# Performance work log

Measured on AMD Instinct MI355X. Metric: run time of the kernel, lower is better.

## Reference

```python
import jax, jax.numpy as jnp
import numpy as np

V = 20000; FV = 2000; PV = 31
SE = 400; FE = 50; PE = 5; NE = 5
FR = FE + PE + NE  # 60, field_rep_embed_size
H = 512; HH = H // 2  # decoder hidden, encoder per-direction hidden
B = 32; T = 32; S = 100
TE = 300  # target_lookup dim (hardcoded in module)


def setup_inputs() -> dict:
    key = jax.random.key(0)
    ks = jax.random.split(key, 26)
    g = lambda k, shape, s: (jax.random.normal(k, shape, jnp.float32) * s)
    inp = {}
    inp['sent'] = jax.random.randint(ks[0], (B, T), 0, V)
    inp['value'] = jax.random.randint(ks[1], (B, S), 0, V)
    inp['field'] = jax.random.randint(ks[2], (B, S), 0, FV)
    inp['ppos'] = jax.random.randint(ks[3], (B, S), 0, PV)
    inp['pneg'] = jax.random.randint(ks[4], (B, S), 0, PV)
    inp['batch_size'] = B
    inp['value_mask'] = jnp.ones((B, S), jnp.float32)
    inp['align_prob'] = jax.random.uniform(ks[5], (B, S, V), jnp.float32)
    # embedding tables
    inp['sent_emb'] = g(ks[6], (V, SE), 0.05)
    inp['field_emb'] = g(ks[7], (FV, FE), 0.05)
    inp['ppos_emb'] = g(ks[8], (PV, PE), 0.05)
    inp['pneg_emb'] = g(ks[9], (PV, NE), 0.05)
    inp['target_emb'] = g(ks[10], (V, TE), 0.05)
    # bidirectional encoder LSTM (per-direction hidden HH), torch gate order i,f,g,o
    ein = SE + FR
    inp['Wi_f'] = g(ks[11], (ein, 4 * HH), ein ** -0.5)
    inp['Wh_f'] = g(ks[12], (HH, 4 * HH), HH ** -0.5)
    inp['b_f'] = jnp.zeros((4 * HH,), jnp.float32)
    inp['Wi_b'] = g(ks[13], (ein, 4 * HH), ein ** -0.5)
    inp['Wh_b'] = g(ks[14], (HH, 4 * HH), HH ** -0.5)
    inp['b_b'] = jnp.zeros((4 * HH,), jnp.float32)
    # decoder LSTM cell + dual attention params
    inp['Wi_d'] = g(ks[15], (SE, 4 * H), SE ** -0.5)
    inp['Wh_d'] = g(ks[16], (H, 4 * H), H ** -0.5)
    inp['b_d'] = jnp.zeros((4 * H,), jnp.float32)
    inp['Wa'] = g(ks[17], (H, H), H ** -0.5)   # encoder-state attention proj
    inp['Wf'] = g(ks[18], (FR, H), FR ** -0.5) # field-rep attention proj
    inp['Wo'] = g(ks[19], (2 * H, H), (2 * H) ** -0.5)  # output proj [h;ctx]
    inp['Wl'] = g(ks[20], (2 * H + SE, 1), (2 * H + SE) ** -0.5)  # lamda gate
    inp['bl'] = jnp.zeros((1,), jnp.float32)
    # linear_out: encoder_hidden_size -> vocab
    inp['Wout'] = g(ks[21], (H, V), H ** -0.5)
    inp['bout'] = jnp.zeros((V,), jnp.float32)
    return inp


def _cell(x, h, c, Wi, Wh, b):
    z = x @ Wi + h @ Wh + b
    i, f, g, o = jnp.split(z, 4, axis=-1)
    c = jax.nn.sigmoid(f) * c + jax.nn.sigmoid(i) * jnp.tanh(g)
    h = jax.nn.sigmoid(o) * jnp.tanh(c)
    return h, c


def _run_lstm(xseq, Wi, Wh, b):
    # xseq [B,L,E] -> hs [B,L,Hn], (hT, cT)
    Bn = xseq.shape[0]; Hn = Wh.shape[0]
    init = (jnp.zeros((Bn, Hn), xseq.dtype), jnp.zeros((Bn, Hn), xseq.dtype))
    def step(carry, xt):
        h, c = _cell(xt, carry[0], carry[1], Wi, Wh, b)
        return (h, c), h
    (hT, cT), hs = jax.lax.scan(step, init, jnp.swapaxes(xseq, 0, 1))
    return jnp.swapaxes(hs, 0, 1), hT, cT


def reference(sent, value, field, ppos, pneg, batch_size, value_mask, align_prob,
              sent_emb, field_emb, ppos_emb, pneg_emb, target_emb,
              Wi_f, Wh_f, b_f, Wi_b, Wh_b, b_b,
              Wi_d, Wh_d, b_d, Wa, Wf, Wo, Wl, bl, Wout, bout):
    # --- encoder input: word emb of table values + field/pos/neg-pos embs ---
    input_d = sent_emb[value]                                     # [B,S,SE]
    input_z = jnp.concatenate([field_emb[field], ppos_emb[ppos], pneg_emb[pneg]], axis=2)  # [B,S,FR]
    enc_in = jnp.concatenate([input_d, input_z], axis=2)          # [B,S,SE+FR]
    # bidirectional LSTM (dropout is eval-mode identity)
    hs_f, hTf, cTf = _run_lstm(enc_in, Wi_f, Wh_f, b_f)
    hs_b, hTb, cTb = _run_lstm(enc_in[:, ::-1], Wi_b, Wh_b, b_b)
    enc_out = jnp.concatenate([hs_f, hs_b[:, ::-1]], axis=-1)     # [B,S,H]
    h0 = jnp.concatenate([hTf, hTb], axis=-1)                     # [B,H]
    c0 = jnp.concatenate([cTf, cTb], axis=-1)

    # --- dual-attention decoder ---
    x_seq = sent_emb[sent]                                        # [B,T,SE]
    enc_proj = jnp.einsum('bsh,hk->bsk', enc_out, Wa)             # word-level keys
    z_proj = jnp.einsum('bsf,fk->bsk', input_z, Wf)               # field-level keys

    def dstep(carry, xt):
        h, c = _cell(xt, carry[0], carry[1], Wi_d, Wh_d, b_d)
        alpha = jax.nn.softmax(jnp.einsum('bsh,bh->bs', enc_proj, h), axis=-1)
        beta = jax.nn.softmax(jnp.einsum('bsh,bh->bs', z_proj, h), axis=-1)
        g = alpha * beta
        g = g / (jnp.sum(g, axis=-1, keepdims=True) + 1e-9)       # dual attn weights
        ctx = jnp.einsum('bs,bsh->bh', g, enc_out)
        out = jnp.tanh(jnp.concatenate([h, ctx], axis=-1) @ Wo)   # [B,H]
        lam = jax.nn.sigmoid(jnp.concatenate([h, ctx, xt], axis=-1) @ Wl + bl)  # [B,1]
        return (h, c), (out, g, lam)

    (hT, cT), (outs, attn, lam) = jax.lax.scan(dstep, (h0, c0), jnp.swapaxes(x_seq, 0, 1))
    outs = jnp.swapaxes(outs, 0, 1)   # [B,T,H]
    attn = jnp.swapaxes(attn, 0, 1)   # [B,T,S]
    lam = jnp.swapaxes(lam, 0, 1)     # [B,T,1]

    p_mod = jax.nn.log_softmax(outs @ Wout + bout, axis=2)        # [B,T,V]
    p_lex = jnp.einsum('bts,bsv->btv', attn, align_prob)          # bmm
    p_bias = jax.nn.log_softmax(lam * p_lex + (1.0 - lam) * p_mod, axis=2)

    # position_idx_to_value: vectorized gather replacing the scalar double loop
    max_idx_attn = jnp.argmax(attn, axis=2)                       # [B,T]
    word_idx = jnp.take_along_axis(value, max_idx_attn, axis=1)   # [B,T]
    attn_pred = target_emb[word_idx]                              # [B,T,300]
    decoder_pred = target_emb[jnp.argmax(p_bias, axis=2)]         # [B,T,300]
    return p_bias, (hT, cT), attn_pred, decoder_pred
```

## Files before the change

kernel.cpp:

```cpp
#include <hip/hip_runtime.h>
#include <cstdint>
#include <cstddef>

static constexpr int Bn  = 32;
static constexpr int Tn  = 32;
static constexpr int Sn  = 100;
static constexpr int Vn  = 20000;
static constexpr int SEn = 400;
static constexpr int EINn= 460;
static constexpr int Hn  = 512;
static constexpr int HHn = 256;
static constexpr int TEn = 300;

__device__ __forceinline__ float sigm(float x) { return 1.f / (1.f + expf(-x)); }

__global__ __launch_bounds__(256) void embed_kernel(
    const int* __restrict__ value, const int* __restrict__ field,
    const int* __restrict__ ppos, const int* __restrict__ pneg,
    const int* __restrict__ sent,
    const float* __restrict__ sent_emb, const float* __restrict__ field_emb,
    const float* __restrict__ ppos_emb, const float* __restrict__ pneg_emb,
    float* __restrict__ enc_in, float* __restrict__ x_seq)
{
    int i = blockIdx.x * 256 + threadIdx.x;
    const int total1 = Bn * Sn * EINn;
    if (i < total1) {
        int e = i % EINn, bs = i / EINn;
        float v;
        if (e < SEn)      v = sent_emb[(size_t)value[bs] * SEn + e];
        else if (e < 450) v = field_emb[field[bs] * 50 + (e - 400)];
        else if (e < 455) v = ppos_emb[ppos[bs] * 5 + (e - 450)];
        else              v = pneg_emb[pneg[bs] * 5 + (e - 455)];
        enc_in[i] = v;
    } else {
        int i2 = i - total1;
        if (i2 < Bn * Tn * SEn) {
            int e = i2 % SEn, bt = i2 / SEn;
            x_seq[i2] = sent_emb[(size_t)sent[bt] * SEn + e];
        }
    }
}

__global__ __launch_bounds__(256) void gemm128_kernel(
    const float* __restrict__ A, const float* __restrict__ Bm,
    const float* __restrict__ bias, float* __restrict__ C,
    int M, int N, int K, int lda, int ldb, int ldc)
{
    __shared__ float As[8][128];
    __shared__ float Bs[8][128];
    const int bm = blockIdx.y * 128, bn = blockIdx.x * 128;
    const int tid = threadIdx.x;
    const int tx = tid & 15, ty = tid >> 4;
    const int row0 = ty * 8, col0 = tx * 8;
    float acc[8][8] = {};
    for (int k0 = 0; k0 < K; k0 += 8) {
        #pragma unroll
        for (int i = 0; i < 4; ++i) {
            int idx = tid + 256 * i;
            int m = idx >> 3, kk = idx & 7;
            float v = 0.f;
            if (bm + m < M && k0 + kk < K) v = A[(size_t)(bm + m) * lda + (k0 + kk)];
            As[kk][m] = v;
        }
        #pragma unroll
        for (int i = 0; i < 4; ++i) {
            int idx = tid + 256 * i;
            int kk = idx >> 7, n = idx & 127;
            float v = 0.f;
            if (k0 + kk < K && bn + n < N) v = Bm[(size_t)(k0 + kk) * ldb + (bn + n)];
            Bs[kk][n] = v;
        }
        __syncthreads();
        #pragma unroll
        for (int kk = 0; kk < 8; ++kk) {
            float a[8], b[8];
            #pragma unroll
            for (int i = 0; i < 8; ++i) a[i] = As[kk][row0 + i];
            #pragma unroll
            for (int j = 0; j < 8; ++j) b[j] = Bs[kk][col0 + j];
            #pragma unroll
            for (int i = 0; i < 8; ++i)
                #pragma unroll
                for (int j = 0; j < 8; ++j) acc[i][j] = fmaf(a[i], b[j], acc[i][j]);
        }
        __syncthreads();
    }
    #pragma unroll
    for (int i = 0; i < 8; ++i) {
        int m = bm + row0 + i;
        if (m >= M) continue;
        #pragma unroll
        for (int j = 0; j < 8; ++j) {
            int n = bn + col0 + j;
            if (n < N) {
                float v = acc[i][j];
                if (bias) v += bias[n];
                C[(size_t)m * ldc + n] = v;
            }
        }
    }
}

__global__ __launch_bounds__(1024) void enc_lstm_kernel(
    const float* __restrict__ Xf, const float* __restrict__ Xb,
    const float* __restrict__ Whf, const float* __restrict__ Whb,
    float* __restrict__ enc_out, float* __restrict__ h0, float* __restrict__ c0)
{
    const int b = blockIdx.x >> 1, dir = blockIdx.x & 1;
    const float* __restrict__ X  = dir ? Xb : Xf;
    const float* __restrict__ Wh = dir ? Whb : Whf;
    __shared__ float h_sh[HHn];
    __shared__ float z_sh[4 * HHn];
    const int u = threadIdx.x;
    float c = 0.f;
    if (u < HHn) h_sh[u] = 0.f;
    __syncthreads();
    for (int step = 0; step < Sn; ++step) {
        const int s = dir ? (Sn - 1 - step) : step;
        const float* xrow = X + ((size_t)b * Sn + s) * 1024;
        float z = xrow[u];
        #pragma unroll 4
        for (int k = 0; k < HHn; ++k)
            z = fmaf(h_sh[k], Wh[k * 1024 + u], z);
        z_sh[u] = z;
        __syncthreads();
        if (u < HHn) {
            float zi = z_sh[u], zf = z_sh[HHn + u], zg = z_sh[2 * HHn + u], zo = z_sh[3 * HHn + u];
            c = sigm(zf) * c + sigm(zi) * tanhf(zg);
            float h = sigm(zo) * tanhf(c);
            h_sh[u] = h;
            enc_out[((size_t)b * Sn + s) * Hn + dir * HHn + u] = h;
            if (step == Sn - 1) {
                h0[b * Hn + dir * HHn + u] = h;
                c0[b * Hn + dir * HHn + u] = c;
            }
        }
        __syncthreads();
    }
}

__global__ __launch_bounds__(1024) void dec_lstm_kernel(
    const float* __restrict__ Xd, const float* __restrict__ Whd,
    const float* __restrict__ h0, const float* __restrict__ c0,
    float* __restrict__ h_all, float* __restrict__ hT, float* __restrict__ cT)
{
    const int b = blockIdx.x;
    __shared__ float h_sh[Hn];
    __shared__ float z_sh[4 * Hn];
    const int u = threadIdx.x;
    float c = 0.f;
    if (u < Hn) { h_sh[u] = h0[b * Hn + u]; c = c0[b * Hn + u]; }
    __syncthreads();
    for (int t = 0; t < Tn; ++t) {
        const float* xrow = Xd + ((size_t)b * Tn + t) * 2048;
        float z0 = xrow[u], z1 = xrow[1024 + u];
        #pragma unroll 4
        for (int k = 0; k < Hn; ++k) {
            float hk = h_sh[k];
            z0 = fmaf(hk, Whd[(size_t)k * 2048 + u], z0);
            z1 = fmaf(hk, Whd[(size_t)k * 2048 + 1024 + u], z1);
        }
        z_sh[u] = z0; z_sh[1024 + u] = z1;
        __syncthreads();
        if (u < Hn) {
            float zi = z_sh[u], zf = z_sh[Hn + u], zg = z_sh[2 * Hn + u], zo = z_sh[3 * Hn + u];
            c = sigm(zf) * c + sigm(zi) * tanhf(zg);
            float h = sigm(zo) * tanhf(c);
            h_sh[u] = h;
            h_all[((size_t)b * Tn + t) * Hn + u] = h;
            if (t == Tn - 1) { hT[b * Hn + u] = h; cT[b * Hn + u] = c; }
        }
        __syncthreads();
    }
}

__global__ __launch_bounds__(256) void dec_post_kernel(
    const float* __restrict__ h_all, const float* __restrict__ enc_proj,
    const float* __restrict__ z_proj, const float* __restrict__ enc_out,
    const float* __restrict__ x_seq, const float* __restrict__ Wo,
    const float* __restrict__ Wl, const float* __restrict__ bl,
    const int* __restrict__ value, const float* __restrict__ target_emb,
    float* __restrict__ outs, float* __restrict__ gattn,
    float* __restrict__ lamv, float* __restrict__ attn_pred)
{
    const int bt = blockIdx.x, b = bt >> 5;
    const int tid = threadIdx.x;
    __shared__ float h_sh[Hn];
    __shared__ float sc[2 * Sn];
    __shared__ float g_sh[Sn];
    __shared__ float ctx_sh[Hn];
    __shared__ float red[256];
    __shared__ int smax_sh;

    for (int i = tid; i < Hn; i += 256) h_sh[i] = h_all[(size_t)bt * Hn + i];
    __syncthreads();

    const int wave = tid >> 6, lane = tid & 63;
    for (int s = wave; s < Sn; s += 4) {
        const float* ep = enc_proj + ((size_t)b * Sn + s) * Hn;
        const float* zp = z_proj  + ((size_t)b * Sn + s) * Hn;
        float da = 0.f, db = 0.f;
        for (int j = lane; j < Hn; j += 64) {
            float hv = h_sh[j];
            da = fmaf(ep[j], hv, da);
            db = fmaf(zp[j], hv, db);
        }
        #pragma unroll
        for (int off = 32; off; off >>= 1) {
            da += __shfl_down(da, off);
            db += __shfl_down(db, off);
        }
        if (lane == 0) { sc[s] = da; sc[Sn + s] = db; }
    }
    __syncthreads();

    if (tid == 0) {
        float ma = -1e30f, mb = -1e30f;
        for (int s = 0; s < Sn; ++s) { ma = fmaxf(ma, sc[s]); mb = fmaxf(mb, sc[Sn + s]); }
        float sa = 0.f, sb = 0.f;
        for (int s = 0; s < Sn; ++s) {
            float ea = expf(sc[s] - ma), eb = expf(sc[Sn + s] - mb);
            sc[s] = ea; sc[Sn + s] = eb; sa += ea; sb += eb;
        }
        float gs = 0.f;
        for (int s = 0; s < Sn; ++s) { float g = (sc[s] / sa) * (sc[Sn + s] / sb); g_sh[s] = g; gs += g; }
        float inv = 1.f / (gs + 1e-9f);
        float best = -1.f; int bi = 0;
        for (int s = 0; s < Sn; ++s) {
            float g = g_sh[s] * inv; g_sh[s] = g;
            if (g > best) { best = g; bi = s; }
        }
        smax_sh = bi;
    }
    __syncthreads();

    for (int s = tid; s < Sn; s += 256) gattn[(size_t)bt * Sn + s] = g_sh[s];
    const int word = value[b * Sn + smax_sh];
    for (int e = tid; e < TEn; e += 256)
        attn_pred[(size_t)bt * TEn + e] = target_emb[(size_t)word * TEn + e];

    for (int u = tid; u < Hn; u += 256) {
        float acc = 0.f;
        for (int s = 0; s < Sn; ++s)
            acc = fmaf(g_sh[s], enc_out[((size_t)b * Sn + s) * Hn + u], acc);
        ctx_sh[u] = acc;
    }
    __syncthreads();

    for (int j = tid; j < Hn; j += 256) {
        float acc = 0.f;
        for (int k = 0; k < Hn; ++k) acc = fmaf(h_sh[k], Wo[(size_t)k * Hn + j], acc);
        for (int k = 0; k < Hn; ++k) acc = fmaf(ctx_sh[k], Wo[(size_t)(Hn + k) * Hn + j], acc);
        outs[(size_t)bt * Hn + j] = tanhf(acc);
    }

    float part = 0.f;
    for (int k = tid; k < Hn; k += 256) part = fmaf(h_sh[k], Wl[k], part);
    for (int k = tid; k < Hn; k += 256) part = fmaf(ctx_sh[k], Wl[Hn + k], part);
    const float* xr = x_seq + (size_t)bt * SEn;
    for (int k = tid; k < SEn; k += 256) part = fmaf(xr[k], Wl[2 * Hn + k], part);
    red[tid] = part;
    __syncthreads();
    for (int s2 = 128; s2; s2 >>= 1) {
        if (tid < s2) red[tid] += red[tid + s2];
        __syncthreads();
    }
    if (tid == 0) lamv[bt] = 1.f / (1.f + expf(-(red[0] + bl[0])));
}

__global__ __launch_bounds__(256) void p_lex_kernel(
    const float* __restrict__ gattn, const float* __restrict__ align_prob,
    float* __restrict__ p_lex)
{
    const int b = blockIdx.z, th = blockIdx.y, vc = blockIdx.x;
    const int tid = threadIdx.x;
    __shared__ float gT[Sn][17];
    for (int i = tid; i < Sn * 16; i += 256) {
        int s = i >> 4, tt = i & 15;
        gT[s][tt] = gattn[((size_t)(b * Tn + th * 16 + tt)) * Sn + s];
    }
    __syncthreads();
    const int v0 = vc * 1024 + tid * 4;
    if (v0 >= Vn) return;
    float acc[16][4] = {};
    for (int s = 0; s < Sn; ++s) {
        const float4 a = *(const float4*)(align_prob + ((size_t)b * Sn + s) * Vn + v0);
        #pragma unroll
        for (int tt = 0; tt < 16; ++tt) {
            float g = gT[s][tt];
            acc[tt][0] = fmaf(g, a.x, acc[tt][0]);
            acc[tt][1] = fmaf(g, a.y, acc[tt][1]);
            acc[tt][2] = fmaf(g, a.z, acc[tt][2]);
            acc[tt][3] = fmaf(g, a.w, acc[tt][3]);
        }
    }
    #pragma unroll
    for (int tt = 0; tt < 16; ++tt) {
        float4 o;
        o.x = acc[tt][0]; o.y = acc[tt][1]; o.z = acc[tt][2]; o.w = acc[tt][3];
        *(float4*)(p_lex + ((size_t)(b * Tn + th * 16 + tt)) * Vn + v0) = o;
    }
}

__global__ __launch_bounds__(256) void reduce1_kernel(
    const float* __restrict__ z, float* __restrict__ lse1)
{
    const int r = blockIdx.x, tid = threadIdx.x;
    const float* row = z + (size_t)r * Vn;
    __shared__ float red[256];
    float m = -1e30f;
    for (int v = tid; v < Vn; v += 256) m = fmaxf(m, row[v]);
    red[tid] = m; __syncthreads();
    for (int s = 128; s; s >>= 1) { if (tid < s) red[tid] = fmaxf(red[tid], red[tid + s]); __syncthreads(); }
    m = red[0]; __syncthreads();
    float sum = 0.f;
    for (int v = tid; v < Vn; v += 256) sum += expf(row[v] - m);
    red[tid] = sum; __syncthreads();
    for (int s = 128; s; s >>= 1) { if (tid < s) red[tid] += red[tid + s]; __syncthreads(); }
    if (tid == 0) lse1[r] = m + logf(red[0]);
}

__global__ __launch_bounds__(256) void combine_kernel(
    float* __restrict__ q, const float* __restrict__ p_lex,
    const float* __restrict__ lamv, const float* __restrict__ lse1,
    float* __restrict__ lse2, int* __restrict__ amax)
{
    const int r = blockIdx.x, tid = threadIdx.x;
    const float l = lamv[r], ls1 = lse1[r];
    float* row = q + (size_t)r * Vn;
    const float* pl = p_lex + (size_t)r * Vn;
    __shared__ float rm[256];
    __shared__ int ri[256];
    float m = -1e30f; int mi = 0;
    for (int v = tid; v < Vn; v += 256) {
        float qq = l * pl[v] + (1.f - l) * (row[v] - ls1);
        row[v] = qq;
        if (qq > m) { m = qq; mi = v; }
    }
    rm[tid] = m; ri[tid] = mi; __syncthreads();
    for (int s = 128; s; s >>= 1) {
        if (tid < s) {
            if (rm[tid + s] > rm[tid] || (rm[tid + s] == rm[tid] && ri[tid + s] < ri[tid])) {
                rm[tid] = rm[tid + s]; ri[tid] = ri[tid + s];
            }
        }
        __syncthreads();
    }
    m = rm[0];
    const int best = ri[0];
    __syncthreads();
    float sum = 0.f;
    for (int v = tid; v < Vn; v += 256) sum += expf(row[v] - m);
    rm[tid] = sum; __syncthreads();
    for (int s = 128; s; s >>= 1) { if (tid < s) rm[tid] += rm[tid + s]; __syncthreads(); }
    if (tid == 0) { lse2[r] = m + logf(rm[0]); amax[r] = best; }
}

__global__ __launch_bounds__(256) void finalize_kernel(
    float* __restrict__ pbias, const float* __restrict__ lse2,
    const int* __restrict__ amax, const float* __restrict__ target_emb,
    float* __restrict__ dec_pred)
{
    const int r = blockIdx.x, tid = threadIdx.x;
    const float ls = lse2[r];
    float* row = pbias + (size_t)r * Vn;
    for (int v = tid; v < Vn; v += 256) row[v] -= ls;
    const int wd = amax[r];
    for (int e = tid; e < TEn; e += 256)
        dec_pred[(size_t)r * TEn + e] = target_emb[(size_t)wd * TEn + e];
}

extern "C" void kernel_launch(void* const* d_in, const int* in_sizes, int n_in,
                              void* d_out, int out_size, void* d_ws, size_t ws_size,
                              hipStream_t stream)
{
    const int*   sent       = (const int*)d_in[0];
    const int*   value      = (const int*)d_in[1];
    const int*   field      = (const int*)d_in[2];
    const int*   ppos       = (const int*)d_in[3];
    const int*   pneg       = (const int*)d_in[4];
    const float* align_prob = (const float*)d_in[7];
    const float* sent_emb   = (const float*)d_in[8];
    const float* field_emb  = (const float*)d_in[9];
    const float* ppos_emb   = (const float*)d_in[10];
    const float* pneg_emb   = (const float*)d_in[11];
    const float* target_emb = (const float*)d_in[12];
    const float* Wi_f = (const float*)d_in[13];
    const float* Wh_f = (const float*)d_in[14];
    const float* b_f  = (const float*)d_in[15];
    const float* Wi_b = (const float*)d_in[16];
    const float* Wh_b = (const float*)d_in[17];
    const float* b_b  = (const float*)d_in[18];
    const float* Wi_d = (const float*)d_in[19];
    const float* Wh_d = (const float*)d_in[20];
    const float* b_d  = (const float*)d_in[21];
    const float* Wa   = (const float*)d_in[22];
    const float* Wf   = (const float*)d_in[23];
    const float* Wo   = (const float*)d_in[24];
    const float* Wl   = (const float*)d_in[25];
    const float* bl   = (const float*)d_in[26];
    const float* Wout = (const float*)d_in[27];
    const float* bout = (const float*)d_in[28];

    float* w = (float*)d_ws;
    float* enc_in   = w; w += (size_t)Bn * Sn * EINn;
    float* x_seq    = w; w += (size_t)Bn * Tn * SEn;
    float* Xf       = w; w += (size_t)Bn * Sn * 1024;
    float* Xb       = w; w += (size_t)Bn * Sn * 1024;
    float* Xd       = w; w += (size_t)Bn * Tn * 2048;
    float* enc_out  = w; w += (size_t)Bn * Sn * Hn;
    float* enc_proj = w; w += (size_t)Bn * Sn * Hn;
    float* z_proj   = w; w += (size_t)Bn * Sn * Hn;
    float* h0       = w; w += (size_t)Bn * Hn;
    float* c0       = w; w += (size_t)Bn * Hn;
    float* h_all    = w; w += (size_t)Bn * Tn * Hn;
    float* outs     = w; w += (size_t)Bn * Tn * Hn;
    float* gattn    = w; w += (size_t)Bn * Tn * Sn;
    float* lamv     = w; w += (size_t)Bn * Tn;
    float* p_lex    = w; w += (size_t)Bn * Tn * Vn;
    float* lse1     = w; w += (size_t)Bn * Tn;
    float* lse2     = w; w += (size_t)Bn * Tn;
    int*   amax     = (int*)w;

    float* outp      = (float*)d_out;
    float* pbias     = outp;
    float* hT        = outp + (size_t)20480000;
    float* cT        = hT + Bn * Hn;
    float* attn_pred = cT + Bn * Hn;
    float* dec_pred  = attn_pred + (size_t)Bn * Tn * TEn;

    embed_kernel<<<7350, 256, 0, stream>>>(value, field, ppos, pneg, sent,
        sent_emb, field_emb, ppos_emb, pneg_emb, enc_in, x_seq);

    dim3 gXf(8, 25);
    gemm128_kernel<<<gXf, 256, 0, stream>>>(enc_in, Wi_f, b_f, Xf, 3200, 1024, 460, 460, 1024, 1024);
    gemm128_kernel<<<gXf, 256, 0, stream>>>(enc_in, Wi_b, b_b, Xb, 3200, 1024, 460, 460, 1024, 1024);
    dim3 gXd(16, 8);
    gemm128_kernel<<<gXd, 256, 0, stream>>>(x_seq, Wi_d, b_d, Xd, 1024, 2048, 400, 400, 2048, 2048);

    enc_lstm_kernel<<<64, 1024, 0, stream>>>(Xf, Xb, Wh_f, Wh_b, enc_out, h0, c0);

    dim3 gPr(4, 25);
    gemm128_kernel<<<gPr, 256, 0, stream>>>(enc_out, Wa, nullptr, enc_proj, 3200, 512, 512, 512, 512, 512);
    gemm128_kernel<<<gPr, 256, 0, stream>>>(enc_in + 400, Wf, nullptr, z_proj, 3200, 512, 60, 460, 512, 512);

    dec_lstm_kernel<<<32, 1024, 0, stream>>>(Xd, Wh_d, h0, c0, h_all, hT, cT);

    dec_post_kernel<<<1024, 256, 0, stream>>>(h_all, enc_proj, z_proj, enc_out, x_seq,
        Wo, Wl, bl, value, target_emb, outs, gattn, lamv, attn_pred);

    dim3 gBig(157, 8);
    gemm128_kernel<<<gBig, 256, 0, stream>>>(outs, Wout, bout, pbias, 1024, 20000, 512, 512, 20000, 20000);

    dim3 gPl(20, 2, 32);
    p_lex_kernel<<<gPl, 256, 0, stream>>>(gattn, align_prob, p_lex);

    reduce1_kernel<<<1024, 256, 0, stream>>>(pbias, lse1);
    combine_kernel<<<1024, 256, 0, stream>>>(pbias, p_lex, lamv, lse1, lse2, amax);
    finalize_kernel<<<1024, 256, 0, stream>>>(pbias, lse2, amax, target_emb, dec_pred);

    (void)in_sizes; (void)n_in; (void)out_size; (void)ws_size;
}
```

Before: 4.923 ms.

## Interleave LSTM recurrent weights per unit and split decoder LSTM across blocks

Recurrent weight matrices are transposed once per call into a per-unit float4 layout holding the i,f,g,o gate columns, so each thread computes all four gates of one unit and applies the cell update without a shared-memory gate exchange. Both LSTM kernels drop from 1024 to 256 threads per block. The decoder is spread over two cooperative blocks per batch row that swap h through a global buffer and a grid-wide atomic barrier every step. This adds a transpose kernel, a memset and spin-barrier latency per step, and stores the scratch weights in the p_lex workspace region before that region is written.

```diff
diff --git a/kernel.cpp b/kernel.cpp
--- a/kernel.cpp
+++ b/kernel.cpp
@@ -13,6 +13,12 @@
 static constexpr int TEn = 300;
 
 __device__ __forceinline__ float sigm(float x) { return 1.f / (1.f + expf(-x)); }
+
+__device__ __forceinline__ void fma4(float hk, const float4 w,
+                                     float& zi, float& zf, float& zg, float& zo) {
+    zi = fmaf(hk, w.x, zi); zf = fmaf(hk, w.y, zf);
+    zg = fmaf(hk, w.z, zg); zo = fmaf(hk, w.w, zo);
+}
 
 __global__ __launch_bounds__(256) void embed_kernel(
     const int* __restrict__ value, const int* __restrict__ field,
@@ -41,6 +47,33 @@
     }
 }
 
+__global__ __launch_bounds__(256) void transpose_wh_kernel(
+    const float* __restrict__ Whf, const float* __restrict__ Whb,
+    const float* __restrict__ Whd,
+    float* __restrict__ Whf_t, float* __restrict__ Whb_t, float* __restrict__ Whd_t)
+{
+    int i = blockIdx.x * 256 + threadIdx.x;
+    if (i < 65536) {
+        int k = i >> 8, u = i & 255;
+        const float* p = Whf + (size_t)k * 1024 + u;
+        float4 o;
+        o.x = p[0]; o.y = p[256]; o.z = p[512]; o.w = p[768];
+        *(float4*)(Whf_t + (size_t)i * 4) = o;
+        p = Whb + (size_t)k * 1024 + u;
+        o.x = p[0]; o.y = p[256]; o.z = p[512]; o.w = p[768];
+        *(float4*)(Whb_t + (size_t)i * 4) = o;
+    } else {
+        int j = i - 65536;
+        if (j < 262144) {
+            int k = j >> 9, u = j & 511;
+            const float* p = Whd + (size_t)k * 2048 + u;
+            float4 o;
+            o.x = p[0]; o.y = p[512]; o.z = p[1024]; o.w = p[1536];
+            *(float4*)(Whd_t + (size_t)j * 4) = o;
+        }
+    }
+}
+
 __global__ __launch_bounds__(256) void gemm128_kernel(
     const float* __restrict__ A, const float* __restrict__ Bm,
     const float* __restrict__ bias, float* __restrict__ C,
@@ -101,75 +134,93 @@
     }
 }
 
-__global__ __launch_bounds__(1024) void enc_lstm_kernel(
+__global__ __launch_bounds__(256) void enc_lstm2_kernel(
     const float* __restrict__ Xf, const float* __restrict__ Xb,
-    const float* __restrict__ Whf, const float* __restrict__ Whb,
+    const float4* __restrict__ Whf_t, const float4* __restrict__ Whb_t,
     float* __restrict__ enc_out, float* __restrict__ h0, float* __restrict__ c0)
 {
     const int b = blockIdx.x >> 1, dir = blockIdx.x & 1;
-    const float* __restrict__ X  = dir ? Xb : Xf;
-    const float* __restrict__ Wh = dir ? Whb : Whf;
-    __shared__ float h_sh[HHn];
-    __shared__ float z_sh[4 * HHn];
+    const float* __restrict__ X = dir ? Xb : Xf;
+    const float4* __restrict__ W = dir ? Whb_t : Whf_t;
+    __shared__ __align__(16) float h_sh[HHn];
     const int u = threadIdx.x;
     float c = 0.f;
-    if (u < HHn) h_sh[u] = 0.f;
+    h_sh[u] = 0.f;
     __syncthreads();
     for (int step = 0; step < Sn; ++step) {
         const int s = dir ? (Sn - 1 - step) : step;
-        const float* xrow = X + ((size_t)b * Sn + s) * 1024;
-        float z = xrow[u];
+        const float* xr = X + ((size_t)(b * Sn + s)) * 1024;
+        float zi = xr[u], zf = xr[256 + u], zg = xr[512 + u], zo = xr[768 + u];
         #pragma unroll 4
-        for (int k = 0; k < HHn; ++k)
-            z = fmaf(h_sh[k], Wh[k * 1024 + u], z);
-        z_sh[u] = z;
-        __syncthreads();
-        if (u < HHn) {
-            float zi = z_sh[u], zf = z_sh[HHn + u], zg = z_sh[2 * HHn + u], zo = z_sh[3 * HHn + u];
-            c = sigm(zf) * c + sigm(zi) * tanhf(zg);
-            float h = sigm(zo) * tanhf(c);
-            h_sh[u] = h;
-            enc_out[((size_t)b * Sn + s) * Hn + dir * HHn + u] = h;
-            if (step == Sn - 1) {
-                h0[b * Hn + dir * HHn + u] = h;
-                c0[b * Hn + dir * HHn + u] = c;
-            }
-        }
-        __syncthreads();
-    }
-}
-
-__global__ __launch_bounds__(1024) void dec_lstm_kernel(
-    const float* __restrict__ Xd, const float* __restrict__ Whd,
+        for (int k4 = 0; k4 < 64; ++k4) {
+            const float4 hv = *(const float4*)&h_sh[k4 << 2];
+            const float4 w0 = W[((k4 << 2) + 0) * 256 + u];
+            const float4 w1 = W[((k4 << 2) + 1) * 256 + u];
+            const float4 w2 = W[((k4 << 2) + 2) * 256 + u];
+            const float4 w3 = W[((k4 << 2) + 3) * 256 + u];
+            fma4(hv.x, w0, zi, zf, zg, zo);
+            fma4(hv.y, w1, zi, zf, zg, zo);
+            fma4(hv.z, w2, zi, zf, zg, zo);
+            fma4(hv.w, w3, zi, zf, zg, zo);
+        }
+        c = sigm(zf) * c + sigm(zi) * tanhf(zg);
+        float h = sigm(zo) * tanhf(c);
+        __syncthreads();
+        h_sh[u] = h;
+        enc_out[((size_t)(b * Sn + s)) * Hn + dir * HHn + u] = h;
+        if (step == Sn - 1) {
+            h0[b * Hn + dir * HHn + u] = h;
+            c0[b * Hn + dir * HHn + u] = c;
+        }
+        __syncthreads();
+    }
+}
+
+__global__ __launch_bounds__(256) void dec_lstm2_kernel(
+    const float* __restrict__ Xd, const float4* __restrict__ Whd_t,
     const float* __restrict__ h0, const float* __restrict__ c0,
-    float* __restrict__ h_all, float* __restrict__ hT, float* __restrict__ cT)
-{
-    const int b = blockIdx.x;
-    __shared__ float h_sh[Hn];
-    __shared__ float z_sh[4 * Hn];
-    const int u = threadIdx.x;
-    float c = 0.f;
-    if (u < Hn) { h_sh[u] = h0[b * Hn + u]; c = c0[b * Hn + u]; }
+    float* __restrict__ h_all, float* __restrict__ hT, float* __restrict__ cT,
+    float* __restrict__ hbuf, int* __restrict__ bar)
+{
+    const int b = blockIdx.x >> 1;
+    const int tid = threadIdx.x;
+    const int u = ((blockIdx.x & 1) << 8) + tid;
+    __shared__ __align__(16) float h_sh[Hn];
+    h_sh[tid]       = h0[b * Hn + tid];
+    h_sh[tid + 256] = h0[b * Hn + 256 + tid];
+    float c = c0[b * Hn + u];
     __syncthreads();
     for (int t = 0; t < Tn; ++t) {
-        const float* xrow = Xd + ((size_t)b * Tn + t) * 2048;
-        float z0 = xrow[u], z1 = xrow[1024 + u];
+        const float* xr = Xd + ((size_t)(b * Tn + t)) * 2048;
+        float zi = xr[u], zf = xr[512 + u], zg = xr[1024 + u], zo = xr[1536 + u];
         #pragma unroll 4
-        for (int k = 0; k < Hn; ++k) {
-            float hk = h_sh[k];
-            z0 = fmaf(hk, Whd[(size_t)k * 2048 + u], z0);
-            z1 = fmaf(hk, Whd[(size_t)k * 2048 + 1024 + u], z1);
-        }
-        z_sh[u] = z0; z_sh[1024 + u] = z1;
-        __syncthreads();
-        if (u < Hn) {
-            float zi = z_sh[u], zf = z_sh[Hn + u], zg = z_sh[2 * Hn + u], zo = z_sh[3 * Hn + u];
-            c = sigm(zf) * c + sigm(zi) * tanhf(zg);
-            float h = sigm(zo) * tanhf(c);
-            h_sh[u] = h;
-            h_all[((size_t)b * Tn + t) * Hn + u] = h;
-            if (t == Tn - 1) { hT[b * Hn + u] = h; cT[b * Hn + u] = c; }
-        }
+        for (int k4 = 0; k4 < 128; ++k4) {
+            const float4 hv = *(const float4*)&h_sh[k4 << 2];
+            const float4 w0 = Whd_t[((k4 << 2) + 0) * 512 + u];
+            const float4 w1 = Whd_t[((k4 << 2) + 1) * 512 + u];
+            const float4 w2 = Whd_t[((k4 << 2) + 2) * 512 + u];
+            const float4 w3 = Whd_t[((k4 << 2) + 3) * 512 + u];
+            fma4(hv.x, w0, zi, zf, zg, zo);
+            fma4(hv.y, w1, zi, zf, zg, zo);
+            fma4(hv.z, w2, zi, zf, zg, zo);
+            fma4(hv.w, w3, zi, zf, zg, zo);
+        }
+        c = sigm(zf) * c + sigm(zi) * tanhf(zg);
+        float h = sigm(zo) * tanhf(c);
+        h_all[((size_t)(b * Tn + t)) * Hn + u] = h;
+        if (t == Tn - 1) { hT[b * Hn + u] = h; cT[b * Hn + u] = c; }
+        __hip_atomic_store(&hbuf[b * Hn + u], h, __ATOMIC_RELEASE, __HIP_MEMORY_SCOPE_AGENT);
+        __syncthreads();
+        if (t == Tn - 1) break;
+        if (tid == 0) {
+            __hip_atomic_fetch_add(bar, 1, __ATOMIC_ACQ_REL, __HIP_MEMORY_SCOPE_AGENT);
+            const int target = 64 * (t + 1);
+            while (__hip_atomic_load(bar, __ATOMIC_ACQUIRE, __HIP_MEMORY_SCOPE_AGENT) < target)
+                __builtin_amdgcn_s_sleep(8);
+        }
+        __syncthreads();
+        h_sh[tid]       = __hip_atomic_load(&hbuf[b * Hn + tid],       __ATOMIC_ACQUIRE, __HIP_MEMORY_SCOPE_AGENT);
+        h_sh[tid + 256] = __hip_atomic_load(&hbuf[b * Hn + 256 + tid], __ATOMIC_ACQUIRE, __HIP_MEMORY_SCOPE_AGENT);
         __syncthreads();
     }
 }
@@ -422,6 +473,12 @@
     float* lse2     = w; w += (size_t)Bn * Tn;
     int*   amax     = (int*)w;
 
+    float* Whf_t = p_lex;
+    float* Whb_t = p_lex + 262144;
+    float* Whd_t = p_lex + 524288;
+    float* hbuf  = p_lex + 2000000;
+    int*   bar   = (int*)(p_lex + 2100000);
+
     float* outp      = (float*)d_out;
     float* pbias     = outp;
     float* hT        = outp + (size_t)20480000;
@@ -431,6 +488,7 @@
 
     embed_kernel<<<7350, 256, 0, stream>>>(value, field, ppos, pneg, sent,
         sent_emb, field_emb, ppos_emb, pneg_emb, enc_in, x_seq);
+    transpose_wh_kernel<<<1280, 256, 0, stream>>>(Wh_f, Wh_b, Wh_d, Whf_t, Whb_t, Whd_t);
 
     dim3 gXf(8, 25);
     gemm128_kernel<<<gXf, 256, 0, stream>>>(enc_in, Wi_f, b_f, Xf, 3200, 1024, 460, 460, 1024, 1024);
@@ -438,13 +496,21 @@
     dim3 gXd(16, 8);
     gemm128_kernel<<<gXd, 256, 0, stream>>>(x_seq, Wi_d, b_d, Xd, 1024, 2048, 400, 400, 2048, 2048);
 
-    enc_lstm_kernel<<<64, 1024, 0, stream>>>(Xf, Xb, Wh_f, Wh_b, enc_out, h0, c0);
+    enc_lstm2_kernel<<<64, 256, 0, stream>>>(Xf, Xb, (const float4*)Whf_t,
+        (const float4*)Whb_t, enc_out, h0, c0);
 
     dim3 gPr(4, 25);
     gemm128_kernel<<<gPr, 256, 0, stream>>>(enc_out, Wa, nullptr, enc_proj, 3200, 512, 512, 512, 512, 512);
     gemm128_kernel<<<gPr, 256, 0, stream>>>(enc_in + 400, Wf, nullptr, z_proj, 3200, 512, 60, 460, 512, 512);
 
-    dec_lstm_kernel<<<32, 1024, 0, stream>>>(Xd, Wh_d, h0, c0, h_all, hT, cT);
+    hipMemsetAsync(bar, 0, 64, stream);
+    {
+        void* args[] = { (void*)&Xd, (void*)&Whd_t, (void*)&h0, (void*)&c0,
+                         (void*)&h_all, (void*)&hT, (void*)&cT,
+                         (void*)&hbuf, (void*)&bar };
+        hipLaunchCooperativeKernel((const void*)dec_lstm2_kernel,
+                                   dim3(64), dim3(256), args, 0, stream);
+    }
 
     dec_post_kernel<<<1024, 256, 0, stream>>>(h_all, enc_proj, z_proj, enc_out, x_seq,
         Wo, Wl, bl, value, target_emb, outs, gattn, lamv, attn_pred);
```

Result: faster. 4.200 ms (-14.7%).
